# Kernel tuning notes

Measured on AMD Instinct MI355X. Metric: run time of the kernel, lower is better.

Reference implementation:

```python
import jax, jax.numpy as jnp
import numpy as np
from jax import lax

D_MODEL = 512
INPUT_DIM = 64
D_INNER = 1024      # expand * d_model
D_STATE = 128
NHEADS = 16         # d_inner // headdim (headdim = ssm_state//num_heads = 64)
HEADDIM = 64
D_CONV = 4
CONV_DIM = D_INNER + 2 * D_STATE          # 1280 (ngroups=1)
D_IN_PROJ = 2 * D_INNER + 2 * D_STATE + NHEADS  # 2320
BATCH = 2
SEQ = 1024
MASK_RATIO = 0.75
EPS = 1e-5


def setup_inputs() -> dict:
    key = jax.random.key(0)
    ks = jax.random.split(key, 14)
    s = lambda fan: 1.0 / np.sqrt(fan)
    return {
        "x": jax.random.normal(ks[0], (BATCH, SEQ, INPUT_DIM), jnp.float32),
        "conv_emb_w": jax.random.normal(ks[1], (D_MODEL, INPUT_DIM, 3), jnp.float32) * s(INPUT_DIM * 3),
        "conv_emb_b": jax.random.normal(ks[2], (D_MODEL,), jnp.float32) * 0.02,
        "cls_token": jax.random.normal(ks[3], (1, 1, D_MODEL), jnp.float32) * 0.02,
        "in_proj_w": jax.random.normal(ks[4], (D_IN_PROJ, D_MODEL), jnp.float32) * s(D_MODEL),
        "conv1d_w": jax.random.normal(ks[5], (CONV_DIM, 1, D_CONV), jnp.float32) * s(D_CONV),
        "conv1d_b": jax.random.normal(ks[6], (CONV_DIM,), jnp.float32) * 0.02,
        "dt_bias": jax.random.uniform(ks[7], (NHEADS,), jnp.float32, -4.0, 0.0),
        "A_log": jnp.log(jax.random.uniform(ks[8], (NHEADS,), jnp.float32, 1.0, 16.0)),
        "D": jax.random.normal(ks[9], (NHEADS,), jnp.float32),
        "rms_w": jnp.ones((D_INNER,), jnp.float32),
        "out_proj_w": jax.random.normal(ks[10], (D_MODEL, D_INNER), jnp.float32) * s(D_INNER),
        "ln_g": jnp.ones((D_MODEL,), jnp.float32),
        "ln_b": jnp.zeros((D_MODEL,), jnp.float32),
    }


def _forward(x, conv_emb_w, conv_emb_b, cls_token, in_proj_w, conv1d_w, conv1d_b,
             dt_bias, A_log, D, rms_w, out_proj_w, ln_g, ln_b):
    b = x.shape[0]
    # ---- conv embedding: Conv1d(k=3, pad=1) over time ----
    xe = lax.conv_general_dilated(x.transpose(0, 2, 1), conv_emb_w, (1,), [(1, 1)],
                                  dimension_numbers=("NCH", "OIH", "NCH"))
    xe = (xe + conv_emb_b[None, :, None]).transpose(0, 2, 1)  # (b, L, d_model)
    # ---- append CLS token at end ----
    h = jnp.concatenate([xe, jnp.broadcast_to(cls_token, (b, 1, D_MODEL))], axis=1)
    L = h.shape[1]
    # ---- Mamba2 block ----
    zxbcdt = jnp.einsum("bld,ed->ble", h, in_proj_w)  # (b, L, 2320)
    z = zxbcdt[..., :D_INNER]
    xBC = zxbcdt[..., D_INNER:D_INNER + CONV_DIM]
    dt = jax.nn.softplus(zxbcdt[..., -NHEADS:] + dt_bias)  # (b, L, h)
    # causal depthwise conv (pad left d_conv-1) + SiLU
    xBC = lax.conv_general_dilated(xBC.transpose(0, 2, 1), conv1d_w, (1,), [(D_CONV - 1, 0)],
                                   dimension_numbers=("NCH", "OIH", "NCH"),
                                   feature_group_count=CONV_DIM)
    xBC = jax.nn.silu((xBC + conv1d_b[None, :, None]).transpose(0, 2, 1))  # (b, L, 1280)
    x_in = xBC[..., :D_INNER].reshape(b, L, NHEADS, HEADDIM)   # (b, L, h, p)
    B = xBC[..., D_INNER:D_INNER + D_STATE]                     # (b, L, n)
    C = xBC[..., D_INNER + D_STATE:]                            # (b, L, n)
    A = -jnp.exp(A_log)                                         # (h,)
    dA = jnp.exp(dt * A)                                        # (b, L, h)
    # selective state-space scan; state (b, h, p, n)
    def step(state, inp):
        x_t, dt_t, B_t, C_t, dA_t = inp  # (b,h,p) (b,h) (b,n) (b,n) (b,h)
        state = state * dA_t[:, :, None, None] + \
            (dt_t[:, :, None] * x_t)[..., None] * B_t[:, None, None, :]
        y_t = jnp.einsum("bhpn,bn->bhp", state, C_t)
        return state, y_t
    s0 = jnp.zeros((b, NHEADS, HEADDIM, D_STATE), x.dtype)
    _, ys = lax.scan(step, s0, (x_in.transpose(1, 0, 2, 3), dt.transpose(1, 0, 2),
                                B.transpose(1, 0, 2), C.transpose(1, 0, 2),
                                dA.transpose(1, 0, 2)))
    y = ys.transpose(1, 0, 2, 3) + D[None, None, :, None] * x_in  # (b, L, h, p)
    y = y.reshape(b, L, D_INNER)
    # gated RMSNorm: gate first, then normalize
    y = y * jax.nn.silu(z)
    y = y * lax.rsqrt(jnp.mean(y * y, axis=-1, keepdims=True) + EPS) * rms_w
    out = jnp.einsum("ble,de->bld", y, out_proj_w)  # (b, L, d_model)
    # ---- LayerNorm ----
    mu = jnp.mean(out, axis=-1, keepdims=True)
    var = jnp.mean((out - mu) ** 2, axis=-1, keepdims=True)
    out = (out - mu) * lax.rsqrt(var + EPS) * ln_g + ln_b
    return out


def reference(x, conv_emb_w, conv_emb_b, cls_token, in_proj_w, conv1d_w, conv1d_b,
              dt_bias, A_log, D, rms_w, out_proj_w, ln_g, ln_b):
    out = _forward(x, conv_emb_w, conv_emb_b, cls_token, in_proj_w, conv1d_w, conv1d_b,
                   dt_bias, A_log, D, rms_w, out_proj_w, ln_g, ln_b)
    b = out.shape[0]
    cls = out[:, -1:, :]
    body = out[:, :-1, :]                      # (b, SEQ, d)
    len_keep = int(SEQ * (1 - MASK_RATIO))     # 256
    noise = jax.random.uniform(jax.random.fold_in(jax.random.key(0), 1), (b, SEQ))
    ids_shuffle = jnp.argsort(noise, axis=1)
    ids_restore = jnp.argsort(ids_shuffle, axis=1)
    ids_keep = ids_shuffle[:, :len_keep]
    x_masked = jnp.take_along_axis(body, ids_keep[:, :, None], axis=1)
    mask = jnp.where(jnp.arange(SEQ)[None, :] < len_keep, 0.0, 1.0)
    mask = jnp.take_along_axis(jnp.broadcast_to(mask, (b, SEQ)), ids_restore, axis=1)
    x_out = jnp.concatenate([x_masked, cls], axis=1)  # (b, len_keep+1, d)
    return (x_out, mask, ids_restore, ids_keep)
```

## Files before the change

kernel.cpp:

```cpp
#include <hip/hip_runtime.h>
#include <hip/hip_bf16.h>
#include <stdint.h>

#define LTOK  1025
#define NROWS 2050
#define DM    512
#define DIN   1024
#define DST   128
#define NHEAD 16
#define HDIM  64
#define CDIM  1280
#define EPROJ 2320
#define QC    64
#define NCH   17

#define O_RIDX   0
#define O_CB     1024
#define O_CLS    1536
#define O_C1B    2048
#define O_DTB    3328
#define O_ALOG   3344
#define O_DV     3360
#define O_RMSW   3376
#define O_LNG    4400
#define O_LNB    4912
#define O_CW     5440
#define O_IPW    103744
#define O_OPW    1291584
#define O_C1W    1815872
#define O_CX     1820992
#define O_ZX     1952064
#define O_XBC    6708064
#define O_DT     9332064
#define O_LGA    9364864
#define O_Y      9397664
#define O_X3     10447264
#define O_OUTG   11496864
#define O_SL     11760032
#define O_CLA    16216480
#define O_SL2    16251296
#define O_KEEP   18479520
#define O_OUTP   18480128
#define O_CWT    19532800
#define O_W2     19581952
#define O_BIAS2  19804672

#define OO_MASK 263168
#define OO_IDR  265216
#define OO_IDK  267264

typedef __attribute__((ext_vector_type(8))) short short8;
typedef __attribute__((ext_vector_type(8))) unsigned short ushortx8;
typedef __attribute__((ext_vector_type(4))) float floatx4;

__device__ __forceinline__ short f2bs(float f) {
  union { float f; uint32_t u; } v; v.f = f;
  uint32_t r = (v.u + 0x7FFFu + ((v.u >> 16) & 1u)) >> 16;
  return (short)r;
}
__device__ __forceinline__ float bf2f(uint16_t u) {
  return __uint_as_float(((uint32_t)u) << 16);
}

struct InPtrs { const void* p[14]; };

__device__ __forceinline__ uint32_t rotl32(uint32_t v, int d) {
  return (v << d) | (v >> (32 - d));
}
__device__ void threefry2x32(uint32_t k0, uint32_t k1, uint32_t c0, uint32_t c1,
                             uint32_t& o0, uint32_t& o1) {
  uint32_t ks0 = k0, ks1 = k1, ks2 = 0x1BD11BDAu ^ k0 ^ k1;
  uint32_t x0 = c0 + ks0, x1 = c1 + ks1;
#define TF_R4(a,b,c,d) \
  x0 += x1; x1 = rotl32(x1,a); x1 ^= x0; \
  x0 += x1; x1 = rotl32(x1,b); x1 ^= x0; \
  x0 += x1; x1 = rotl32(x1,c); x1 ^= x0; \
  x0 += x1; x1 = rotl32(x1,d); x1 ^= x0;
  TF_R4(13,15,26,6)  x0 += ks1; x1 += ks2 + 1u;
  TF_R4(17,29,16,24) x0 += ks2; x1 += ks0 + 2u;
  TF_R4(13,15,26,6)  x0 += ks0; x1 += ks1 + 3u;
  TF_R4(17,29,16,24) x0 += ks1; x1 += ks2 + 4u;
  TF_R4(13,15,26,6)  x0 += ks2; x1 += ks0 + 5u;
#undef TF_R4
  o0 = x0; o1 = x1;
}

__device__ int detect_is_f32(const uint32_t* w, int nelem) {
  int nw = nelem / 2; if (nw > 16) nw = 16;
  int insane = 0, lozero = 0, anynz = 0;
  for (int i = 0; i < nw; ++i) {
    uint32_t word = w[i];
    if (word != 0u) anynz = 1;
    uint32_t lo = word & 0xffffu;
    if (lo == 0u) { lozero++; continue; }
    float v = __uint_as_float(lo << 16);
    float a = fabsf(v);
    if (!(a >= 1e-8f && a <= 1e4f)) insane++;
  }
  if (insane >= 2) return 1;
  if (lozero == nw && anynz) return 1;
  return 0;
}

__global__ __launch_bounds__(256) void k_convert(InPtrs ptrs, float* ws,
                                                 float* out, int* rowidx) {
  static const int sizes[13] = {98304, 512, 512, 1187840, 5120, 1280,
                                16, 16, 16, 1024, 524288, 512, 512};
  static const int offs[13]  = {O_CW, O_CB, O_CLS, O_IPW, O_C1W, O_C1B,
                                O_DTB, O_ALOG, O_DV, O_RMSW, O_OPW, O_LNG, O_LNB};
  static const int isbf[13]  = {1,0,0,1,0,0,0,0,0,0,1,0,0};
  static const int smallT[15] = {1,2,4,4,4,4,4,5,5,6,7,8,9,11,12};
  static const int smallB[15] = {0,0,0,1,2,3,4,0,1,0,0,0,0,0,0};
  int bx = blockIdx.x;
  int tid = threadIdx.x;

  if (bx < 2048) {
    int b = bx >> 10, idx = bx & 1023;
    const uint32_t* xp = (const uint32_t*)ptrs.p[0];
    __shared__ int xf;
    if (tid == 0) xf = detect_is_f32(xp, 131072);
    __syncthreads();
    if (tid < 192) {
      int i = tid / 3, k = tid % 3;
      int tt = idx + k - 1;
      float v = 0.f;
      if (tt >= 0 && tt < 1024) {
        long src = ((long)(b * 1024 + tt)) * 64 + i;
        v = xf ? ((const float*)xp)[src] : bf2f(((const uint16_t*)xp)[src]);
      }
      ((uint16_t*)(ws + O_X3))[((long)(b * 1024 + idx)) * 192 + tid] = (uint16_t)f2bs(v);
    }
    return;
  }
  bx -= 2048;

  int t, blk;
  if (bx < 1160) { t = 3; blk = bx; }
  else {
    bx -= 1160;
    if (bx < 512) { t = 10; blk = bx; }
    else {
      bx -= 512;
      if (bx < 96) {
        const uint32_t* w = (const uint32_t*)ptrs.p[1];
        __shared__ int sf;
        if (tid == 0) sf = detect_is_f32(w, 98304);
        __syncthreads();
        int base = (bx * 256 + tid) * 4;
        if (base >= 98304) return;
        uint16_t vv[4];
        if (sf) {
          const float4 f = *(const float4*)((const float*)w + base);
          vv[0] = (uint16_t)f2bs(f.x); vv[1] = (uint16_t)f2bs(f.y);
          vv[2] = (uint16_t)f2bs(f.z); vv[3] = (uint16_t)f2bs(f.w);
        } else {
          const uint32_t* s = w + (base >> 1);
          uint32_t w0 = s[0], w1 = s[1];
          vv[0] = (uint16_t)(w0 & 0xffffu); vv[1] = (uint16_t)(w0 >> 16);
          vv[2] = (uint16_t)(w1 & 0xffffu); vv[3] = (uint16_t)(w1 >> 16);
        }
        int o = base / 192, ik = base % 192;
        uint16_t* cwt = (uint16_t*)(ws + O_CWT);
#pragma unroll
        for (int j = 0; j < 4; ++j)
          cwt[(long)(ik + j) * 512 + o] = vv[j];
        return;
      }
      bx -= 96;
      if (bx < 32) {
        int seg = bx & 15, b = bx >> 4;
        uint8_t* keep = (uint8_t*)(ws + O_KEEP);
        __shared__ float vals[1024];
        uint32_t fk0, fk1;
        threefry2x32(0u, 0u, 0u, 1u, fk0, fk1);
#pragma unroll
        for (int k = 0; k < 4; ++k) {
          int i = tid + k * 256;
          uint32_t o0, o1;
          threefry2x32(fk0, fk1, 0u, (uint32_t)(b * 1024 + i), o0, o1);
          uint32_t bits = o0 ^ o1;
          vals[i] = __uint_as_float((bits >> 9) | 0x3f800000u) - 1.0f;
        }
        __syncthreads();
        int tg = seg * 64 + (tid >> 2);
        int qq = tid & 3;
        float v = vals[tg];
        int r = 0;
        int j0 = qq * 256;
        for (int it = 0; it < 256; ++it) {
          int j = j0 + ((it + qq * 8) & 255);
          float vj = vals[j];
          r += (vj < v || (vj == v && j < tg)) ? 1 : 0;
        }
        r += __shfl_xor(r, 1, 64);
        r += __shfl_xor(r, 2, 64);
        if (qq == 0) {
          out[OO_IDR + b * 1024 + tg] = (float)r;
          out[OO_MASK + b * 1024 + tg] = (r < 256) ? 0.0f : 1.0f;
          keep[b * LTOK + tg] = (r < 256) ? 1 : 0;
          if (r < 256) {
            out[OO_IDK + b * 256 + r] = (float)tg;
            rowidx[b * 257 + r] = b * LTOK + tg;
          }
          if (tg == 0) {
            rowidx[b * 257 + 256] = b * LTOK + 1024;
            keep[b * LTOK + 1024] = 1;
          }
        }
        return;
      }
      bx -= 32;
      if (bx >= 15) return;
      t = smallT[bx]; blk = smallB[bx];
    }
  }

  int n = sizes[t];
  const uint32_t* w = (const uint32_t*)ptrs.p[t + 1];
  __shared__ int sf;
  if (tid == 0) sf = detect_is_f32(w, n);
  __syncthreads();
  int base = (blk * 256 + tid) * 4;
  if (base >= n) return;
  if (isbf[t]) {
    ushort4 o;
    if (sf) {
      const float4 vv = *(const float4*)((const float*)w + base);
      o.x = (uint16_t)f2bs(vv.x); o.y = (uint16_t)f2bs(vv.y);
      o.z = (uint16_t)f2bs(vv.z); o.w = (uint16_t)f2bs(vv.w);
    } else {
      const uint32_t* s = w + (base >> 1);
      uint32_t w0 = s[0], w1 = s[1];
      o.x = (uint16_t)(w0 & 0xffffu); o.y = (uint16_t)(w0 >> 16);
      o.z = (uint16_t)(w1 & 0xffffu); o.w = (uint16_t)(w1 >> 16);
    }
    *(ushort4*)((uint16_t*)(ws + offs[t]) + base) = o;
  } else {
    float* dst = ws + offs[t];
    if (sf) {
      *(float4*)(dst + base) = *(const float4*)((const float*)w + base);
    } else {
      const uint32_t* s = w + (base >> 1);
      uint32_t w0 = s[0], w1 = s[1];
      float4 o;
      o.x = __uint_as_float((w0 & 0xffffu) << 16);
      o.y = __uint_as_float(w0 & 0xffff0000u);
      o.z = __uint_as_float((w1 & 0xffffu) << 16);
      o.w = __uint_as_float(w1 & 0xffff0000u);
      *(float4*)(dst + base) = o;
    }
  }
}

__global__ __launch_bounds__(256) void k_w2(const uint16_t* __restrict__ IPW,
                                            const uint16_t* __restrict__ CWT,
                                            const float* __restrict__ cb,
                                            const float* __restrict__ cls,
                                            uint16_t* __restrict__ W2,
                                            float* __restrict__ bias2,
                                            uint16_t* __restrict__ ZX) {
  int bx = blockIdx.x;
  int tid = threadIdx.x;

  if (bx >= 111) {
    __shared__ float scb[512];
    __shared__ float scl[512];
    for (int i = tid; i < 512; i += 256) {
      scb[i] = cb[i];
      scl[i] = bf2f((uint16_t)f2bs(cls[i]));
    }
    __syncthreads();
    int e = (bx - 111) * 232 + tid;
    if (tid < 232 && e < 2320) {
      float sb = 0.f, sc = 0.f;
      for (int d8 = 0; d8 < 512; d8 += 8) {
        ushortx8 v = *(const ushortx8*)(IPW + (long)e * 512 + d8);
#pragma unroll
        for (int j = 0; j < 8; ++j) {
          float wv = bf2f(v[j]);
          sb = fmaf(wv, scb[d8 + j], sb);
          sc = fmaf(wv, scl[d8 + j], sc);
        }
      }
      bias2[e] = sb;
      uint16_t cz = (uint16_t)f2bs(sc);
      ZX[(long)1024 * EPROJ + e] = cz;
      ZX[(long)2049 * EPROJ + e] = cz;
    }
    return;
  }

  int bm = bx / 3, bn = bx % 3;
  __shared__ __align__(16) short sA[64 * 136];
  __shared__ __align__(16) short sB[64 * 136];
  int lane = tid & 63, w = tid >> 6, lm = lane & 15, q = lane >> 4;

  floatx4 acc[4] = {};
  for (int ph = 0; ph < 4; ++ph) {
    int d0 = ph * 128;
#pragma unroll
    for (int it = 0; it < 4; ++it) {
      int li = it * 256 + tid;
      int row = li >> 4, col = (li & 15) * 8;
      int ge = bm * 64 + row;
      ushortx8 av = {0,0,0,0,0,0,0,0};
      if (ge < 2320) av = *(const ushortx8*)(IPW + (long)ge * 512 + d0 + col);
      *(ushortx8*)&sA[row * 136 + col] = av;
      ushortx8 bv = *(const ushortx8*)(CWT + (long)(bn * 64 + row) * 512 + d0 + col);
      *(ushortx8*)&sB[row * 136 + col] = bv;
    }
    __syncthreads();
#pragma unroll
    for (int kk = 0; kk < 4; ++kk) {
      short8 a = *(const short8*)&sA[(w * 16 + lm) * 136 + kk * 32 + q * 8];
#pragma unroll
      for (int ct = 0; ct < 4; ++ct) {
        short8 b = *(const short8*)&sB[(ct * 16 + lm) * 136 + kk * 32 + q * 8];
        acc[ct] = __builtin_amdgcn_mfma_f32_16x16x32_bf16(a, b, acc[ct], 0, 0, 0);
      }
    }
    __syncthreads();
  }
#pragma unroll
  for (int reg = 0; reg < 4; ++reg) {
    int e = bm * 64 + w * 16 + q * 4 + reg;
    if (e < 2320) {
#pragma unroll
      for (int ct = 0; ct < 4; ++ct)
        W2[(long)e * 192 + bn * 64 + ct * 16 + lm] = (uint16_t)f2bs(acc[ct][reg]);
    }
  }
}

__global__ __launch_bounds__(256) void k_ipgemm(const uint16_t* __restrict__ X3,
                                                const uint16_t* __restrict__ W2,
                                                const float* __restrict__ bias2,
                                                uint16_t* __restrict__ ZX) {
  __shared__ __align__(16) short sA[64 * 200];
  __shared__ __align__(16) short sB[64 * 200];
  int tid = threadIdx.x;
  int lane = tid & 63, w = tid >> 6, lm = lane & 15, q = lane >> 4;
  int bm = blockIdx.y * 64, bn = blockIdx.x * 64;

#pragma unroll
  for (int it = 0; it < 6; ++it) {
    int li = it * 256 + tid;
    int row = li / 24, col = (li % 24) * 8;
    ushortx8 av = *(const ushortx8*)(X3 + (long)(bm + row) * 192 + col);
    *(ushortx8*)&sA[row * 200 + col] = av;
    int gn = bn + row;
    ushortx8 bv = {0,0,0,0,0,0,0,0};
    if (gn < 2320) bv = *(const ushortx8*)(W2 + (long)gn * 192 + col);
    *(ushortx8*)&sB[row * 200 + col] = bv;
  }
  __syncthreads();

  floatx4 acc[4] = {};
#pragma unroll
  for (int kb = 0; kb < 6; ++kb) {
    short8 a = *(const short8*)&sA[(w * 16 + lm) * 200 + kb * 32 + q * 8];
#pragma unroll
    for (int ct = 0; ct < 4; ++ct) {
      short8 b = *(const short8*)&sB[(ct * 16 + lm) * 200 + kb * 32 + q * 8];
      acc[ct] = __builtin_amdgcn_mfma_f32_16x16x32_bf16(a, b, acc[ct], 0, 0, 0);
    }
  }
#pragma unroll
  for (int reg = 0; reg < 4; ++reg) {
    int r = bm + w * 16 + q * 4 + reg;
    long crow = (long)((r >> 10) * LTOK + (r & 1023));
#pragma unroll
    for (int ct = 0; ct < 4; ++ct) {
      int e = bn + ct * 16 + lm;
      if (e < 2320)
        ZX[crow * EPROJ + e] = (uint16_t)f2bs(acc[ct][reg] + bias2[e]);
    }
  }
}

__global__ __launch_bounds__(256) void k_conv1d(const uint16_t* __restrict__ zx,
                                                const float* __restrict__ w,
                                                const float* __restrict__ bias,
                                                uint16_t* __restrict__ xbc,
                                                const float* __restrict__ dtb,
                                                const float* __restrict__ alog,
                                                float* __restrict__ dt,
                                                float* __restrict__ lga) {
  long rp_ = blockIdx.x;
  if (rp_ >= NROWS) {
    int idx = (int)(rp_ - NROWS) * 256 + threadIdx.x;
    if (idx < NROWS * NHEAD) {
      int rr = idx >> 4, h = idx & 15;
      float xv = bf2f(zx[(long)rr * EPROJ + (EPROJ - NHEAD) + h]) + dtb[h];
      float dtv = (xv > 20.f) ? xv : log1pf(expf(xv));
      dt[idx] = dtv;
      lga[idx] = dtv * (-expf(alog[h]));
    }
    return;
  }
  {
    int xcd = (int)(rp_ & 7), slot = (int)(rp_ >> 3);
    rp_ = (xcd < 2) ? (long)xcd * 257 + slot
                    : (long)514 + (long)(xcd - 2) * 256 + slot;
  }
  long r = rp_;
  int b = (int)(r / LTOK), t = (int)(r % LTOK);
  for (int c4 = threadIdx.x * 4; c4 < CDIM; c4 += 1024) {
    float4 bi = *(const float4*)(bias + c4);
    float a0 = bi.x, a1 = bi.y, a2 = bi.z, a3 = bi.w;
    float4 w0 = *(const float4*)(w + (c4 + 0) * 4);
    float4 w1 = *(const float4*)(w + (c4 + 1) * 4);
    float4 w2 = *(const float4*)(w + (c4 + 2) * 4);
    float4 w3 = *(const float4*)(w + (c4 + 3) * 4);
    float wr0[4] = {w0.x, w0.y, w0.z, w0.w};
    float wr1[4] = {w1.x, w1.y, w1.z, w1.w};
    float wr2[4] = {w2.x, w2.y, w2.z, w2.w};
    float wr3[4] = {w3.x, w3.y, w3.z, w3.w};
#pragma unroll
    for (int k = 0; k < 4; ++k) {
      int tt = t - 3 + k;
      if (tt >= 0) {
        ushort4 xv = *(const ushort4*)(zx + ((long)(b * LTOK + tt)) * EPROJ + DIN + c4);
        a0 = fmaf(wr0[k], bf2f(xv.x), a0);
        a1 = fmaf(wr1[k], bf2f(xv.y), a1);
        a2 = fmaf(wr2[k], bf2f(xv.z), a2);
        a3 = fmaf(wr3[k], bf2f(xv.w), a3);
      }
    }
    ushort4 o;
    o.x = (uint16_t)f2bs(a0 / (1.f + expf(-a0)));
    o.y = (uint16_t)f2bs(a1 / (1.f + expf(-a1)));
    o.z = (uint16_t)f2bs(a2 / (1.f + expf(-a2)));
    o.w = (uint16_t)f2bs(a3 / (1.f + expf(-a3)));
    *(ushort4*)(xbc + r * CDIM + c4) = o;
  }
}

__global__ __launch_bounds__(256) void k_ssd1(const uint16_t* __restrict__ xbc,
                                              const float* __restrict__ dt,
                                              const float* __restrict__ lga,
                                              float* __restrict__ SL,
                                              float* __restrict__ CLA) {
  int blk = blockIdx.x;
  int c = blk % NCH;
  int hh = blk / NCH;
  int h = hh & 15, b = hh >> 4;
  int tid = threadIdx.x;
  int lane = tid & 63, w = tid >> 6;
  int lm = lane & 15, q = lane >> 4;

  __shared__ __align__(16) short sBT[128 * 72];
  __shared__ __align__(16) short sXT[64 * 72];
  __shared__ float wwv[64];

  int t0 = c * QC;
  const uint16_t* base = xbc + (long)b * LTOK * CDIM;

  if (tid < 64) {
    int t = t0 + tid;
    float dtv = (t < LTOK) ? dt[((long)(b * LTOK + t)) * NHEAD + h] : 0.f;
    float v   = (t < LTOK) ? lga[((long)(b * LTOK + t)) * NHEAD + h] : 0.f;
#pragma unroll
    for (int off = 1; off < 64; off <<= 1) {
      float u = __shfl_up(v, off, 64);
      if (lane >= off) v += u;
    }
    float clEnd = __shfl(v, 63, 64);
    wwv[tid] = __expf(clEnd - v) * dtv;
    CLA[(long)blk * 64 + tid] = v;
  }
  __syncthreads();

#pragma unroll
  for (int k = 0; k < 8; ++k) {
    int e4 = (tid + k * 256) * 4;
    int row = e4 >> 7, col = e4 & 127;
    int t = t0 + row;
    ushort4 bv = {0,0,0,0};
    if (t < LTOK) bv = *(const ushort4*)(base + (long)t * CDIM + DIN + col);
    float wv = wwv[row];
    sBT[(col  )*72+row]=f2bs(bf2f(bv.x)*wv); sBT[(col+1)*72+row]=f2bs(bf2f(bv.y)*wv);
    sBT[(col+2)*72+row]=f2bs(bf2f(bv.z)*wv); sBT[(col+3)*72+row]=f2bs(bf2f(bv.w)*wv);
  }
#pragma unroll
  for (int k = 0; k < 4; ++k) {
    int e4 = (tid + k * 256) * 4;
    int row = e4 >> 6, col = e4 & 63;
    int t = t0 + row;
    ushort4 xv = {0,0,0,0};
    if (t < LTOK) xv = *(const ushort4*)(base + (long)t * CDIM + h * 64 + col);
    sXT[(col  )*72+row]=(short)xv.x; sXT[(col+1)*72+row]=(short)xv.y;
    sXT[(col+2)*72+row]=(short)xv.z; sXT[(col+3)*72+row]=(short)xv.w;
  }
  __syncthreads();

  floatx4 s[2][4] = {};
#pragma unroll
  for (int kb = 0; kb < 2; ++kb) {
    short8 bfr[4];
#pragma unroll
    for (int ct = 0; ct < 4; ++ct)
      bfr[ct] = *(const short8*)&sXT[(ct*16 + lm)*72 + kb*32 + q*8];
#pragma unroll
    for (int nt = 0; nt < 2; ++nt) {
      short8 a = *(const short8*)&sBT[((w*2+nt)*16 + lm)*72 + kb*32 + q*8];
#pragma unroll
      for (int ct = 0; ct < 4; ++ct)
        s[nt][ct] = __builtin_amdgcn_mfma_f32_16x16x32_bf16(a, bfr[ct], s[nt][ct], 0, 0, 0);
    }
  }
  float* slp = SL + (long)blk * 8192;
#pragma unroll
  for (int nt = 0; nt < 2; ++nt)
#pragma unroll
    for (int ct = 0; ct < 4; ++ct)
#pragma unroll
      for (int reg = 0; reg < 4; ++reg) {
        int n = (w*2+nt)*16 + q*4 + reg;
        int p = ct*16 + lm;
        slp[n*64 + p] = s[nt][ct][reg];
      }
}

__global__ __launch_bounds__(256) void k_comb(const float* __restrict__ SL,
                                              const float* __restrict__ CLA,
                                              uint16_t* __restrict__ SL2) {
  int bx = blockIdx.x;
  int piece = bx & 15;
  int hh = bx >> 4;
  int off = piece * 512 + threadIdx.x * 2;
  long cb0 = (long)hh * NCH;
  float P[NCH];
  float2 tmp[NCH];
#pragma unroll
  for (int c = 0; c < NCH; ++c) {
    P[c] = __expf(CLA[(cb0 + c) * 64 + 63]);
    tmp[c] = *(const float2*)(SL + (cb0 + c) * 8192 + off);
  }
  float2 s = make_float2(0.f, 0.f);
#pragma unroll
  for (int c = 0; c < NCH; ++c) {
    uint32_t packed = (uint32_t)(uint16_t)f2bs(s.x) | ((uint32_t)(uint16_t)f2bs(s.y) << 16);
    *(uint32_t*)(SL2 + (cb0 + c) * 8192 + off) = packed;
    s.x = fmaf(P[c], s.x, tmp[c].x);
    s.y = fmaf(P[c], s.y, tmp[c].y);
  }
}

__global__ __launch_bounds__(256) void k_ssd3(const uint16_t* __restrict__ xbc,
                                              const float* __restrict__ dt,
                                              const uint16_t* __restrict__ SL2,
                                              const float* __restrict__ CLA,
                                              const uint8_t* __restrict__ keepf,
                                              float* __restrict__ Y) {
  int blk = blockIdx.x;
  int c = blk % NCH;
  int hh = blk / NCH;
  int h = hh & 15, b = hh >> 4;
  int tid = threadIdx.x;
  int lane = tid & 63, w = tid >> 6;
  int lm = lane & 15, q = lane >> 4;

  __shared__ __align__(16) short sST[64 * 136];
  __shared__ __align__(16) short sXT[64 * 72];
  __shared__ __align__(16) short sM[64 * 72];
  __shared__ float dtw[64], clA[64], evec[64];
  __shared__ uint8_t kf[64];

  int t0 = c * QC;
  const uint16_t* base = xbc + (long)b * LTOK * CDIM;
  const uint16_t* slp = SL2 + (long)blk * 8192;

  if (tid < 64) {
    int t = t0 + tid;
    dtw[tid] = (t < LTOK) ? dt[((long)(b * LTOK + t)) * NHEAD + h] : 0.f;
    float v = CLA[(long)blk * 64 + tid];
    clA[tid] = v;
    evec[tid] = __expf(v);
    kf[tid] = (t < LTOK) ? keepf[b * LTOK + t] : 0;
  }

#pragma unroll
  for (int k = 0; k < 4; ++k) {
    int e4 = (tid + k * 256) * 4;
    int row = e4 >> 6, col = e4 & 63;
    int t = t0 + row;
    ushort4 xv = {0,0,0,0};
    if (t < LTOK) xv = *(const ushort4*)(base + (long)t * CDIM + h * 64 + col);
    sXT[(col  )*72+row]=(short)xv.x; sXT[(col+1)*72+row]=(short)xv.y;
    sXT[(col+2)*72+row]=(short)xv.z; sXT[(col+3)*72+row]=(short)xv.w;
  }
#pragma unroll
  for (int k = 0; k < 8; ++k) {
    int e4 = (tid + k * 256) * 4;
    int n = e4 >> 6, p = e4 & 63;
    ushort4 sv = *(const ushort4*)(slp + n * 64 + p);
    sST[(p  )*136+n]=(short)sv.x; sST[(p+1)*136+n]=(short)sv.y;
    sST[(p+2)*136+n]=(short)sv.z; sST[(p+3)*136+n]=(short)sv.w;
  }
  __syncthreads();

  short8 cfr[4];
  int tA = t0 + w*16 + lm;
  bool tAok = tA < LTOK;
#pragma unroll
  for (int kb = 0; kb < 4; ++kb) {
    short8 z = {0,0,0,0,0,0,0,0};
    cfr[kb] = tAok ? *(const short8*)(base + (long)tA * CDIM + DIN + DST + kb*32 + q*8) : z;
  }

  floatx4 g[4] = {};
#pragma unroll
  for (int kb = 0; kb < 4; ++kb) {
#pragma unroll
    for (int ct = 0; ct < 4; ++ct) {
      int tB = t0 + ct*16 + lm;
      short8 z = {0,0,0,0,0,0,0,0};
      short8 bb = (tB < LTOK) ? *(const short8*)(base + (long)tB * CDIM + DIN + kb*32 + q*8) : z;
      g[ct] = __builtin_amdgcn_mfma_f32_16x16x32_bf16(cfr[kb], bb, g[ct], 0, 0, 0);
    }
  }
#pragma unroll
  for (int ct = 0; ct < 4; ++ct) {
    int tp = ct*16 + lm;
#pragma unroll
    for (int reg = 0; reg < 4; ++reg) {
      int tl = w*16 + q*4 + reg;
      float m = 0.f;
      if (tp <= tl) m = g[ct][reg] * __expf(clA[tl] - clA[tp]) * dtw[tp];
      sM[tl*72 + tp] = f2bs(m);
    }
  }
  floatx4 y2[4] = {};
#pragma unroll
  for (int kb = 0; kb < 4; ++kb) {
#pragma unroll
    for (int ct = 0; ct < 4; ++ct) {
      short8 bb = *(const short8*)&sST[(ct*16 + lm)*136 + kb*32 + q*8];
      y2[ct] = __builtin_amdgcn_mfma_f32_16x16x32_bf16(cfr[kb], bb, y2[ct], 0, 0, 0);
    }
  }
  __syncthreads();
  floatx4 y1[4] = {};
#pragma unroll
  for (int kb = 0; kb < 2; ++kb) {
    short8 a = *(const short8*)&sM[(w*16 + lm)*72 + kb*32 + q*8];
#pragma unroll
    for (int ct = 0; ct < 4; ++ct) {
      short8 bb = *(const short8*)&sXT[(ct*16 + lm)*72 + kb*32 + q*8];
      y1[ct] = __builtin_amdgcn_mfma_f32_16x16x32_bf16(a, bb, y1[ct], 0, 0, 0);
    }
  }
#pragma unroll
  for (int reg = 0; reg < 4; ++reg) {
    int tl = w*16 + q*4 + reg;
    int t = t0 + tl;
    if (t < LTOK && kf[tl]) {
      float ev = evec[tl];
#pragma unroll
      for (int ct = 0; ct < 4; ++ct) {
        int p = ct*16 + lm;
        Y[((long)(b * LTOK + t)) * DIN + h * 64 + p] = y1[ct][reg] + ev * y2[ct][reg];
      }
    }
  }
}

__global__ __launch_bounds__(256) void k_gaterms(const float* __restrict__ Y,
                                                 const uint16_t* __restrict__ xbc,
                                                 const uint16_t* __restrict__ zx,
                                                 const float* __restrict__ Dv,
                                                 const float* __restrict__ rmsw,
                                                 const int* __restrict__ ridx,
                                                 uint16_t* __restrict__ G) {
  int rr = blockIdx.x;
  long r = ridx[rr];
  int tid = threadIdx.x;
  int e = tid * 4;
  int h = tid >> 4;
  float4 a = *(const float4*)(Y + r * DIN + e);
  const ushort4 xu = *(const ushort4*)(xbc + r * CDIM + e);
  const ushort4 zu = *(const ushort4*)(zx + r * EPROJ + e);
  float Dh = Dv[h];
  float y0 = a.x + Dh * bf2f(xu.x), y1 = a.y + Dh * bf2f(xu.y);
  float y2 = a.z + Dh * bf2f(xu.z), y3 = a.w + Dh * bf2f(xu.w);
  float z0 = bf2f(zu.x), z1 = bf2f(zu.y), z2 = bf2f(zu.z), z3 = bf2f(zu.w);
  float g0 = y0 * (z0 / (1.f + expf(-z0)));
  float g1 = y1 * (z1 / (1.f + expf(-z1)));
  float g2 = y2 * (z2 / (1.f + expf(-z2)));
  float g3 = y3 * (z3 / (1.f + expf(-z3)));
  __shared__ float red[256];
  red[tid] = g0*g0 + g1*g1 + g2*g2 + g3*g3;
  __syncthreads();
  for (int st = 128; st; st >>= 1) {
    if (tid < st) red[tid] += red[tid + st];
    __syncthreads();
  }
  float scale = rsqrtf(red[0] * (1.0f / 1024.0f) + 1e-5f);
  float4 rw = *(const float4*)(rmsw + e);
  ushort4 o;
  o.x = (uint16_t)f2bs(g0 * scale * rw.x);
  o.y = (uint16_t)f2bs(g1 * scale * rw.y);
  o.z = (uint16_t)f2bs(g2 * scale * rw.z);
  o.w = (uint16_t)f2bs(g3 * scale * rw.w);
  *(ushort4*)(G + (long)rr * DIN + e) = o;
}

__global__ __launch_bounds__(256) void k_ogemm(const uint16_t* __restrict__ A,
                                               const uint16_t* __restrict__ Bw,
                                               float* __restrict__ OUTP) {
  __shared__ __align__(16) short sA[64 * 264];
  __shared__ __align__(16) short sB[64 * 264];
  int tid = threadIdx.x;
  int lane = tid & 63, w = tid >> 6;
  int lm = lane & 15, q = lane >> 4;
  int bm = blockIdx.y * 64, bn = blockIdx.x * 64;
  int kbase = blockIdx.z * 256;

#pragma unroll
  for (int it = 0; it < 8; ++it) {
    int li = it * 256 + tid;
    int row = li >> 5, col = (li & 31) * 8;
    int gm = bm + row;
    ushortx8 av = {0,0,0,0,0,0,0,0};
    if (gm < 514) av = *(const ushortx8*)(A + (long)gm * 1024 + kbase + col);
    *(ushortx8*)&sA[row * 264 + col] = av;
    ushortx8 bv = *(const ushortx8*)(Bw + (long)(bn + row) * 1024 + kbase + col);
    *(ushortx8*)&sB[row * 264 + col] = bv;
  }
  __syncthreads();

  floatx4 acc[4] = {};
#pragma unroll
  for (int kb = 0; kb < 8; ++kb) {
    short8 a = *(const short8*)&sA[(w * 16 + lm) * 264 + kb * 32 + q * 8];
#pragma unroll
    for (int ct = 0; ct < 4; ++ct) {
      short8 b = *(const short8*)&sB[(ct * 16 + lm) * 264 + kb * 32 + q * 8];
      acc[ct] = __builtin_amdgcn_mfma_f32_16x16x32_bf16(a, b, acc[ct], 0, 0, 0);
    }
  }
  float* op = OUTP + (long)blockIdx.z * 263168;
#pragma unroll
  for (int reg = 0; reg < 4; ++reg) {
    int r = bm + w * 16 + q * 4 + reg;
    if (r < 514) {
#pragma unroll
      for (int ct = 0; ct < 4; ++ct)
        op[(long)r * 512 + bn + ct * 16 + lm] = acc[ct][reg];
    }
  }
}

__global__ __launch_bounds__(256) void k_ln(const float* __restrict__ outp,
                                            const float* __restrict__ lng,
                                            const float* __restrict__ lnb,
                                            float* __restrict__ out) {
  int r = blockIdx.x;
  int tid = threadIdx.x;
  long e = (long)r * DM + tid * 2;
  float2 v0 = *(const float2*)(outp + e);
  float2 v1 = *(const float2*)(outp + 263168 + e);
  float2 v2 = *(const float2*)(outp + 2 * 263168 + e);
  float2 v3 = *(const float2*)(outp + 3 * 263168 + e);
  float2 v;
  v.x = ((v0.x + v1.x) + v2.x) + v3.x;
  v.y = ((v0.y + v1.y) + v2.y) + v3.y;
  __shared__ float red[256];
  red[tid] = v.x + v.y;
  __syncthreads();
  for (int st = 128; st; st >>= 1) { if (tid < st) red[tid] += red[tid + st]; __syncthreads(); }
  float mu = red[0] * (1.0f / 512.0f);
  __syncthreads();
  float dx = v.x - mu, dy = v.y - mu;
  red[tid] = dx * dx + dy * dy;
  __syncthreads();
  for (int st = 128; st; st >>= 1) { if (tid < st) red[tid] += red[tid + st]; __syncthreads(); }
  float sc = rsqrtf(red[0] * (1.0f / 512.0f) + 1e-5f);
  int c = tid * 2;
  out[(long)r * DM + c]     = dx * sc * lng[c] + lnb[c];
  out[(long)r * DM + c + 1] = dy * sc * lng[c + 1] + lnb[c + 1];
}

extern "C" void kernel_launch(void* const* d_in, const int* in_sizes, int n_in,
                              void* d_out, int out_size, void* d_ws, size_t ws_size,
                              hipStream_t stream) {
  float* ws = (float*)d_ws;
  float* out = (float*)d_out;
  int* rowidx = (int*)(ws + O_RIDX);
  InPtrs ip;
  for (int i = 0; i < 14; ++i) ip.p[i] = d_in[i];

  hipLaunchKernelGGL(k_convert, dim3(3863), dim3(256), 0, stream, ip, ws, out, rowidx);
  hipLaunchKernelGGL(k_w2, dim3(121), dim3(256), 0, stream,
                     (const uint16_t*)(ws + O_IPW), (const uint16_t*)(ws + O_CWT),
                     ws + O_CB, ws + O_CLS,
                     (uint16_t*)(ws + O_W2), ws + O_BIAS2, (uint16_t*)(ws + O_ZX));
  hipLaunchKernelGGL(k_ipgemm, dim3(37, 32), dim3(256), 0, stream,
                     (const uint16_t*)(ws + O_X3), (const uint16_t*)(ws + O_W2),
                     ws + O_BIAS2, (uint16_t*)(ws + O_ZX));
  hipLaunchKernelGGL(k_conv1d, dim3(2179), dim3(256), 0, stream,
                     (const uint16_t*)(ws + O_ZX), ws + O_C1W, ws + O_C1B,
                     (uint16_t*)(ws + O_XBC),
                     ws + O_DTB, ws + O_ALOG, ws + O_DT, ws + O_LGA);
  hipLaunchKernelGGL(k_ssd1, dim3(32 * NCH), dim3(256), 0, stream,
                     (const uint16_t*)(ws + O_XBC), ws + O_DT, ws + O_LGA,
                     ws + O_SL, ws + O_CLA);
  hipLaunchKernelGGL(k_comb, dim3(512), dim3(256), 0, stream,
                     ws + O_SL, ws + O_CLA, (uint16_t*)(ws + O_SL2));
  hipLaunchKernelGGL(k_ssd3, dim3(32 * NCH), dim3(256), 0, stream,
                     (const uint16_t*)(ws + O_XBC), ws + O_DT,
                     (const uint16_t*)(ws + O_SL2), ws + O_CLA,
                     (const uint8_t*)(ws + O_KEEP), ws + O_Y);
  hipLaunchKernelGGL(k_gaterms, dim3(514), dim3(256), 0, stream,
                     ws + O_Y, (const uint16_t*)(ws + O_XBC),
                     (const uint16_t*)(ws + O_ZX), ws + O_DV, ws + O_RMSW,
                     (const int*)rowidx, (uint16_t*)(ws + O_X3));
  hipLaunchKernelGGL(k_ogemm, dim3(8, 9, 4), dim3(256), 0, stream,
                     (const uint16_t*)(ws + O_X3), (const uint16_t*)(ws + O_OPW),
                     ws + O_OUTP);
  hipLaunchKernelGGL(k_ln, dim3(514), dim3(256), 0, stream,
                     ws + O_OUTP, ws + O_LNG, ws + O_LNB, out);
}
```

Measured before the change: 191.1 us.

## Fuse input/weight dtype conversion into consuming GEMM loads, shrink convert kernel

Stops converting in_proj, out_proj weights and building the im2col X3 buffer in the convert kernel. Instead the w2, input-projection GEMM and output GEMM kernels read the raw inputs and convert to bf16 on load. The conv-embedding weight transpose is permuted so the im2col column order matches contiguous 8-element loads. This removes thousands of convert blocks and a round trip through workspace, at the cost of every block re-running the dtype detection and, with f32 inputs, reading twice the bytes per GEMM tile.

```diff
diff --git a/kernel.cpp b/kernel.cpp
--- a/kernel.cpp
+++ b/kernel.cpp
@@ -102,6 +102,22 @@
   return 0;
 }
 
+__device__ __forceinline__ ushortx8 load8_bf16(const void* src, long idx, int isf32) {
+  ushortx8 r;
+  if (isf32) {
+    const float* p = (const float*)src + idx;
+    float4 f0 = *(const float4*)p;
+    float4 f1 = *(const float4*)(p + 4);
+    r[0] = (uint16_t)f2bs(f0.x); r[1] = (uint16_t)f2bs(f0.y);
+    r[2] = (uint16_t)f2bs(f0.z); r[3] = (uint16_t)f2bs(f0.w);
+    r[4] = (uint16_t)f2bs(f1.x); r[5] = (uint16_t)f2bs(f1.y);
+    r[6] = (uint16_t)f2bs(f1.z); r[7] = (uint16_t)f2bs(f1.w);
+  } else {
+    r = *(const ushortx8*)((const uint16_t*)src + idx);
+  }
+  return r;
+}
+
 __global__ __launch_bounds__(256) void k_convert(InPtrs ptrs, float* ws,
                                                  float* out, int* rowidx) {
   static const int sizes[13] = {98304, 512, 512, 1187840, 5120, 1280,
@@ -114,106 +130,80 @@
   int bx = blockIdx.x;
   int tid = threadIdx.x;
 
-  if (bx < 2048) {
-    int b = bx >> 10, idx = bx & 1023;
-    const uint32_t* xp = (const uint32_t*)ptrs.p[0];
-    __shared__ int xf;
-    if (tid == 0) xf = detect_is_f32(xp, 131072);
+  if (bx < 96) {
+    const uint32_t* w = (const uint32_t*)ptrs.p[1];
+    __shared__ int sf;
+    if (tid == 0) sf = detect_is_f32(w, 98304);
     __syncthreads();
-    if (tid < 192) {
-      int i = tid / 3, k = tid % 3;
-      int tt = idx + k - 1;
-      float v = 0.f;
-      if (tt >= 0 && tt < 1024) {
-        long src = ((long)(b * 1024 + tt)) * 64 + i;
-        v = xf ? ((const float*)xp)[src] : bf2f(((const uint16_t*)xp)[src]);
+    int base = (bx * 256 + tid) * 4;
+    if (base >= 98304) return;
+    uint16_t vv[4];
+    if (sf) {
+      const float4 f = *(const float4*)((const float*)w + base);
+      vv[0] = (uint16_t)f2bs(f.x); vv[1] = (uint16_t)f2bs(f.y);
+      vv[2] = (uint16_t)f2bs(f.z); vv[3] = (uint16_t)f2bs(f.w);
+    } else {
+      const uint32_t* s = w + (base >> 1);
+      uint32_t w0 = s[0], w1 = s[1];
+      vv[0] = (uint16_t)(w0 & 0xffffu); vv[1] = (uint16_t)(w0 >> 16);
+      vv[2] = (uint16_t)(w1 & 0xffffu); vv[3] = (uint16_t)(w1 >> 16);
+    }
+    int o = base / 192, ik = base % 192;
+    uint16_t* cwt = (uint16_t*)(ws + O_CWT);
+#pragma unroll
+    for (int j = 0; j < 4; ++j) {
+      int ikj = ik + j;
+      int kp = (ikj % 3) * 64 + (ikj / 3);
+      cwt[(long)kp * 512 + o] = vv[j];
+    }
+    return;
+  }
+  bx -= 96;
+  if (bx < 32) {
+    int seg = bx & 15, b = bx >> 4;
+    uint8_t* keep = (uint8_t*)(ws + O_KEEP);
+    __shared__ float vals[1024];
+    uint32_t fk0, fk1;
+    threefry2x32(0u, 0u, 0u, 1u, fk0, fk1);
+#pragma unroll
+    for (int k = 0; k < 4; ++k) {
+      int i = tid + k * 256;
+      uint32_t o0, o1;
+      threefry2x32(fk0, fk1, 0u, (uint32_t)(b * 1024 + i), o0, o1);
+      uint32_t bits = o0 ^ o1;
+      vals[i] = __uint_as_float((bits >> 9) | 0x3f800000u) - 1.0f;
+    }
+    __syncthreads();
+    int tg = seg * 64 + (tid >> 2);
+    int qq = tid & 3;
+    float v = vals[tg];
+    int r = 0;
+    int j0 = qq * 256;
+    for (int it = 0; it < 256; ++it) {
+      int j = j0 + ((it + qq * 8) & 255);
+      float vj = vals[j];
+      r += (vj < v || (vj == v && j < tg)) ? 1 : 0;
+    }
+    r += __shfl_xor(r, 1, 64);
+    r += __shfl_xor(r, 2, 64);
+    if (qq == 0) {
+      out[OO_IDR + b * 1024 + tg] = (float)r;
+      out[OO_MASK + b * 1024 + tg] = (r < 256) ? 0.0f : 1.0f;
+      keep[b * LTOK + tg] = (r < 256) ? 1 : 0;
+      if (r < 256) {
+        out[OO_IDK + b * 256 + r] = (float)tg;
+        rowidx[b * 257 + r] = b * LTOK + tg;
       }
-      ((uint16_t*)(ws + O_X3))[((long)(b * 1024 + idx)) * 192 + tid] = (uint16_t)f2bs(v);
+      if (tg == 0) {
+        rowidx[b * 257 + 256] = b * LTOK + 1024;
+        keep[b * LTOK + 1024] = 1;
+      }
     }
     return;
   }
-  bx -= 2048;
-
-  int t, blk;
-  if (bx < 1160) { t = 3; blk = bx; }
-  else {
-    bx -= 1160;
-    if (bx < 512) { t = 10; blk = bx; }
-    else {
-      bx -= 512;
-      if (bx < 96) {
-        const uint32_t* w = (const uint32_t*)ptrs.p[1];
-        __shared__ int sf;
-        if (tid == 0) sf = detect_is_f32(w, 98304);
-        __syncthreads();
-        int base = (bx * 256 + tid) * 4;
-        if (base >= 98304) return;
-        uint16_t vv[4];
-        if (sf) {
-          const float4 f = *(const float4*)((const float*)w + base);
-          vv[0] = (uint16_t)f2bs(f.x); vv[1] = (uint16_t)f2bs(f.y);
-          vv[2] = (uint16_t)f2bs(f.z); vv[3] = (uint16_t)f2bs(f.w);
-        } else {
-          const uint32_t* s = w + (base >> 1);
-          uint32_t w0 = s[0], w1 = s[1];
-          vv[0] = (uint16_t)(w0 & 0xffffu); vv[1] = (uint16_t)(w0 >> 16);
-          vv[2] = (uint16_t)(w1 & 0xffffu); vv[3] = (uint16_t)(w1 >> 16);
-        }
-        int o = base / 192, ik = base % 192;
-        uint16_t* cwt = (uint16_t*)(ws + O_CWT);
-#pragma unroll
-        for (int j = 0; j < 4; ++j)
-          cwt[(long)(ik + j) * 512 + o] = vv[j];
-        return;
-      }
-      bx -= 96;
-      if (bx < 32) {
-        int seg = bx & 15, b = bx >> 4;
-        uint8_t* keep = (uint8_t*)(ws + O_KEEP);
-        __shared__ float vals[1024];
-        uint32_t fk0, fk1;
-        threefry2x32(0u, 0u, 0u, 1u, fk0, fk1);
-#pragma unroll
-        for (int k = 0; k < 4; ++k) {
-          int i = tid + k * 256;
-          uint32_t o0, o1;
-          threefry2x32(fk0, fk1, 0u, (uint32_t)(b * 1024 + i), o0, o1);
-          uint32_t bits = o0 ^ o1;
-          vals[i] = __uint_as_float((bits >> 9) | 0x3f800000u) - 1.0f;
-        }
-        __syncthreads();
-        int tg = seg * 64 + (tid >> 2);
-        int qq = tid & 3;
-        float v = vals[tg];
-        int r = 0;
-        int j0 = qq * 256;
-        for (int it = 0; it < 256; ++it) {
-          int j = j0 + ((it + qq * 8) & 255);
-          float vj = vals[j];
-          r += (vj < v || (vj == v && j < tg)) ? 1 : 0;
-        }
-        r += __shfl_xor(r, 1, 64);
-        r += __shfl_xor(r, 2, 64);
-        if (qq == 0) {
-          out[OO_IDR + b * 1024 + tg] = (float)r;
-          out[OO_MASK + b * 1024 + tg] = (r < 256) ? 0.0f : 1.0f;
-          keep[b * LTOK + tg] = (r < 256) ? 1 : 0;
-          if (r < 256) {
-            out[OO_IDK + b * 256 + r] = (float)tg;
-            rowidx[b * 257 + r] = b * LTOK + tg;
-          }
-          if (tg == 0) {
-            rowidx[b * 257 + 256] = b * LTOK + 1024;
-            keep[b * LTOK + 1024] = 1;
-          }
-        }
-        return;
-      }
-      bx -= 32;
-      if (bx >= 15) return;
-      t = smallT[bx]; blk = smallB[bx];
-    }
-  }
+  bx -= 32;
+  if (bx >= 15) return;
+  int t = smallT[bx], blk = smallB[bx];
 
   int n = sizes[t];
   const uint32_t* w = (const uint32_t*)ptrs.p[t + 1];
@@ -252,7 +242,7 @@
   }
 }
 
-__global__ __launch_bounds__(256) void k_w2(const uint16_t* __restrict__ IPW,
+__global__ __launch_bounds__(256) void k_w2(const void* __restrict__ IPWr,
                                             const uint16_t* __restrict__ CWT,
                                             const float* __restrict__ cb,
                                             const float* __restrict__ cls,
@@ -261,6 +251,8 @@
                                             uint16_t* __restrict__ ZX) {
   int bx = blockIdx.x;
   int tid = threadIdx.x;
+  __shared__ int sf;
+  if (tid == 0) sf = detect_is_f32((const uint32_t*)IPWr, 1187840);
 
   if (bx >= 111) {
     __shared__ float scb[512];
@@ -274,7 +266,7 @@
     if (tid < 232 && e < 2320) {
       float sb = 0.f, sc = 0.f;
       for (int d8 = 0; d8 < 512; d8 += 8) {
-        ushortx8 v = *(const ushortx8*)(IPW + (long)e * 512 + d8);
+        ushortx8 v = load8_bf16(IPWr, (long)e * 512 + d8, sf);
 #pragma unroll
         for (int j = 0; j < 8; ++j) {
           float wv = bf2f(v[j]);
@@ -294,6 +286,7 @@
   __shared__ __align__(16) short sA[64 * 136];
   __shared__ __align__(16) short sB[64 * 136];
   int lane = tid & 63, w = tid >> 6, lm = lane & 15, q = lane >> 4;
+  __syncthreads();
 
   floatx4 acc[4] = {};
   for (int ph = 0; ph < 4; ++ph) {
@@ -304,7 +297,7 @@
       int row = li >> 4, col = (li & 15) * 8;
       int ge = bm * 64 + row;
       ushortx8 av = {0,0,0,0,0,0,0,0};
-      if (ge < 2320) av = *(const ushortx8*)(IPW + (long)ge * 512 + d0 + col);
+      if (ge < 2320) av = load8_bf16(IPWr, (long)ge * 512 + d0 + col, sf);
       *(ushortx8*)&sA[row * 136 + col] = av;
       ushortx8 bv = *(const ushortx8*)(CWT + (long)(bn * 64 + row) * 512 + d0 + col);
       *(ushortx8*)&sB[row * 136 + col] = bv;
@@ -332,7 +325,7 @@
   }
 }
 
-__global__ __launch_bounds__(256) void k_ipgemm(const uint16_t* __restrict__ X3,
+__global__ __launch_bounds__(256) void k_ipgemm(const void* __restrict__ xraw,
                                                 const uint16_t* __restrict__ W2,
                                                 const float* __restrict__ bias2,
                                                 uint16_t* __restrict__ ZX) {
@@ -341,17 +334,26 @@
   int tid = threadIdx.x;
   int lane = tid & 63, w = tid >> 6, lm = lane & 15, q = lane >> 4;
   int bm = blockIdx.y * 64, bn = blockIdx.x * 64;
+  __shared__ int xf;
+  if (tid == 0) xf = detect_is_f32((const uint32_t*)xraw, 131072);
+  __syncthreads();
 
 #pragma unroll
   for (int it = 0; it < 6; ++it) {
     int li = it * 256 + tid;
-    int row = li / 24, col = (li % 24) * 8;
-    ushortx8 av = *(const ushortx8*)(X3 + (long)(bm + row) * 192 + col);
-    *(ushortx8*)&sA[row * 200 + col] = av;
+    int row = li / 24, colb = (li % 24) * 8;
+    int r = bm + row;
+    int b = r >> 10, idx = r & 1023;
+    int kk = colb >> 6, i0 = colb & 63;
+    int tt = idx + kk - 1;
+    ushortx8 av = {0,0,0,0,0,0,0,0};
+    if (tt >= 0 && tt < 1024)
+      av = load8_bf16(xraw, ((long)(b * 1024 + tt)) * 64 + i0, xf);
+    *(ushortx8*)&sA[row * 200 + colb] = av;
     int gn = bn + row;
     ushortx8 bv = {0,0,0,0,0,0,0,0};
-    if (gn < 2320) bv = *(const ushortx8*)(W2 + (long)gn * 192 + col);
-    *(ushortx8*)&sB[row * 200 + col] = bv;
+    if (gn < 2320) bv = *(const ushortx8*)(W2 + (long)gn * 192 + colb);
+    *(ushortx8*)&sB[row * 200 + colb] = bv;
   }
   __syncthreads();
 
@@ -707,7 +709,7 @@
 }
 
 __global__ __launch_bounds__(256) void k_ogemm(const uint16_t* __restrict__ A,
-                                               const uint16_t* __restrict__ Bw,
+                                               const void* __restrict__ OPWr,
                                                float* __restrict__ OUTP) {
   __shared__ __align__(16) short sA[64 * 264];
   __shared__ __align__(16) short sB[64 * 264];
@@ -716,6 +718,9 @@
   int lm = lane & 15, q = lane >> 4;
   int bm = blockIdx.y * 64, bn = blockIdx.x * 64;
   int kbase = blockIdx.z * 256;
+  __shared__ int of;
+  if (tid == 0) of = detect_is_f32((const uint32_t*)OPWr, 524288);
+  __syncthreads();
 
 #pragma unroll
   for (int it = 0; it < 8; ++it) {
@@ -725,7 +730,7 @@
     ushortx8 av = {0,0,0,0,0,0,0,0};
     if (gm < 514) av = *(const ushortx8*)(A + (long)gm * 1024 + kbase + col);
     *(ushortx8*)&sA[row * 264 + col] = av;
-    ushortx8 bv = *(const ushortx8*)(Bw + (long)(bn + row) * 1024 + kbase + col);
+    ushortx8 bv = load8_bf16(OPWr, (long)(bn + row) * 1024 + kbase + col, of);
     *(ushortx8*)&sB[row * 264 + col] = bv;
   }
   __syncthreads();
@@ -791,13 +796,13 @@
   InPtrs ip;
   for (int i = 0; i < 14; ++i) ip.p[i] = d_in[i];
 
-  hipLaunchKernelGGL(k_convert, dim3(3863), dim3(256), 0, stream, ip, ws, out, rowidx);
+  hipLaunchKernelGGL(k_convert, dim3(143), dim3(256), 0, stream, ip, ws, out, rowidx);
   hipLaunchKernelGGL(k_w2, dim3(121), dim3(256), 0, stream,
-                     (const uint16_t*)(ws + O_IPW), (const uint16_t*)(ws + O_CWT),
+                     (const void*)d_in[4], (const uint16_t*)(ws + O_CWT),
                      ws + O_CB, ws + O_CLS,
                      (uint16_t*)(ws + O_W2), ws + O_BIAS2, (uint16_t*)(ws + O_ZX));
   hipLaunchKernelGGL(k_ipgemm, dim3(37, 32), dim3(256), 0, stream,
-                     (const uint16_t*)(ws + O_X3), (const uint16_t*)(ws + O_W2),
+                     (const void*)d_in[0], (const uint16_t*)(ws + O_W2),
                      ws + O_BIAS2, (uint16_t*)(ws + O_ZX));
   hipLaunchKernelGGL(k_conv1d, dim3(2179), dim3(256), 0, stream,
                      (const uint16_t*)(ws + O_ZX), ws + O_C1W, ws + O_C1B,
@@ -817,7 +822,7 @@
                      (const uint16_t*)(ws + O_ZX), ws + O_DV, ws + O_RMSW,
                      (const int*)rowidx, (uint16_t*)(ws + O_X3));
   hipLaunchKernelGGL(k_ogemm, dim3(8, 9, 4), dim3(256), 0, stream,
-                     (const uint16_t*)(ws + O_X3), (const uint16_t*)(ws + O_OPW),
+                     (const uint16_t*)(ws + O_X3), (const void*)d_in[11],
                      ws + O_OUTP);
   hipLaunchKernelGGL(k_ln, dim3(514), dim3(256), 0, stream,
                      ws + O_OUTP, ws + O_LNG, ws + O_LNB, out);
```

Result: slower. 208.4 us (+9.0%).

## Skip z-gate stores for masked rows and tile conv1d over four timesteps

Applied to the files above, without the earlier changes.

The in-projection GEMM epilogue now reads a per-row keep mask and skips writing the z (gate) columns for rows that are later discarded, which cuts global store traffic. The depthwise conv1d kernel now computes four consecutive timesteps per block and reuses the seven loaded input rows across the 4-tap windows, instead of reloading four rows for every output row. This shrinks the grid from one block per row to one per four rows. The trade-off is more registers per thread and fewer blocks to fill the device.

```diff
diff --git a/kernel.cpp b/kernel.cpp
--- a/kernel.cpp
+++ b/kernel.cpp
@@ -335,13 +335,19 @@
 __global__ __launch_bounds__(256) void k_ipgemm(const uint16_t* __restrict__ X3,
                                                 const uint16_t* __restrict__ W2,
                                                 const float* __restrict__ bias2,
+                                                const uint8_t* __restrict__ keep,
                                                 uint16_t* __restrict__ ZX) {
   __shared__ __align__(16) short sA[64 * 200];
   __shared__ __align__(16) short sB[64 * 200];
+  __shared__ uint8_t skp[64];
   int tid = threadIdx.x;
   int lane = tid & 63, w = tid >> 6, lm = lane & 15, q = lane >> 4;
   int bm = blockIdx.y * 64, bn = blockIdx.x * 64;
 
+  if (tid < 64) {
+    int rr = bm + tid;
+    skp[tid] = keep[(rr >> 10) * LTOK + (rr & 1023)];
+  }
 #pragma unroll
   for (int it = 0; it < 6; ++it) {
     int li = it * 256 + tid;
@@ -369,10 +375,11 @@
   for (int reg = 0; reg < 4; ++reg) {
     int r = bm + w * 16 + q * 4 + reg;
     long crow = (long)((r >> 10) * LTOK + (r & 1023));
+    int kp = skp[r - bm];
 #pragma unroll
     for (int ct = 0; ct < 4; ++ct) {
       int e = bn + ct * 16 + lm;
-      if (e < 2320)
+      if (e < 2320 && (e >= DIN || kp))
         ZX[crow * EPROJ + e] = (uint16_t)f2bs(acc[ct][reg] + bias2[e]);
     }
   }
@@ -386,9 +393,10 @@
                                                 const float* __restrict__ alog,
                                                 float* __restrict__ dt,
                                                 float* __restrict__ lga) {
-  long rp_ = blockIdx.x;
-  if (rp_ >= NROWS) {
-    int idx = (int)(rp_ - NROWS) * 256 + threadIdx.x;
+  int g = blockIdx.x;
+  int tid = threadIdx.x;
+  if (g >= 514) {
+    int idx = (g - 514) * 256 + tid;
     if (idx < NROWS * NHEAD) {
       int rr = idx >> 4, h = idx & 15;
       float xv = bf2f(zx[(long)rr * EPROJ + (EPROJ - NHEAD) + h]) + dtb[h];
@@ -399,40 +407,55 @@
     return;
   }
   {
-    int xcd = (int)(rp_ & 7), slot = (int)(rp_ >> 3);
-    rp_ = (xcd < 2) ? (long)xcd * 257 + slot
-                    : (long)514 + (long)(xcd - 2) * 256 + slot;
-  }
-  long r = rp_;
-  int b = (int)(r / LTOK), t = (int)(r % LTOK);
-  for (int c4 = threadIdx.x * 4; c4 < CDIM; c4 += 1024) {
+    int xcd = g & 7, slot = g >> 3;
+    g = (xcd < 2) ? xcd * 65 + slot : 130 + (xcd - 2) * 64 + slot;
+  }
+  int b = g / 257, gi = g % 257;
+  int t0 = gi * 4;
+  int nr = (t0 == 1024) ? 1 : 4;
+  const uint16_t* zrow = zx + (long)b * LTOK * EPROJ + DIN;
+  for (int c4 = tid * 4; c4 < CDIM; c4 += 1024) {
     float4 bi = *(const float4*)(bias + c4);
-    float a0 = bi.x, a1 = bi.y, a2 = bi.z, a3 = bi.w;
     float4 w0 = *(const float4*)(w + (c4 + 0) * 4);
     float4 w1 = *(const float4*)(w + (c4 + 1) * 4);
     float4 w2 = *(const float4*)(w + (c4 + 2) * 4);
     float4 w3 = *(const float4*)(w + (c4 + 3) * 4);
-    float wr0[4] = {w0.x, w0.y, w0.z, w0.w};
-    float wr1[4] = {w1.x, w1.y, w1.z, w1.w};
-    float wr2[4] = {w2.x, w2.y, w2.z, w2.w};
-    float wr3[4] = {w3.x, w3.y, w3.z, w3.w};
-#pragma unroll
-    for (int k = 0; k < 4; ++k) {
-      int tt = t - 3 + k;
-      if (tt >= 0) {
-        ushort4 xv = *(const ushort4*)(zx + ((long)(b * LTOK + tt)) * EPROJ + DIN + c4);
-        a0 = fmaf(wr0[k], bf2f(xv.x), a0);
-        a1 = fmaf(wr1[k], bf2f(xv.y), a1);
-        a2 = fmaf(wr2[k], bf2f(xv.z), a2);
-        a3 = fmaf(wr3[k], bf2f(xv.w), a3);
+    float wr[4][4] = {{w0.x, w0.y, w0.z, w0.w}, {w1.x, w1.y, w1.z, w1.w},
+                      {w2.x, w2.y, w2.z, w2.w}, {w3.x, w3.y, w3.z, w3.w}};
+    float acc[4][4];
+#pragma unroll
+    for (int ri = 0; ri < 4; ++ri) {
+      acc[ri][0] = bi.x; acc[ri][1] = bi.y; acc[ri][2] = bi.z; acc[ri][3] = bi.w;
+    }
+#pragma unroll
+    for (int dtt = -3; dtt <= 3; ++dtt) {
+      int tt = t0 + dtt;
+      if (tt < 0 || tt > 1024) continue;
+      ushort4 xv = *(const ushort4*)(zrow + (long)tt * EPROJ + c4);
+      float x0 = bf2f(xv.x), x1 = bf2f(xv.y), x2 = bf2f(xv.z), x3 = bf2f(xv.w);
+#pragma unroll
+      for (int ri = 0; ri < 4; ++ri) {
+        int k = dtt - ri + 3;
+        if (k >= 0 && k <= 3) {
+          acc[ri][0] = fmaf(wr[0][k], x0, acc[ri][0]);
+          acc[ri][1] = fmaf(wr[1][k], x1, acc[ri][1]);
+          acc[ri][2] = fmaf(wr[2][k], x2, acc[ri][2]);
+          acc[ri][3] = fmaf(wr[3][k], x3, acc[ri][3]);
+        }
       }
     }
-    ushort4 o;
-    o.x = (uint16_t)f2bs(a0 / (1.f + expf(-a0)));
-    o.y = (uint16_t)f2bs(a1 / (1.f + expf(-a1)));
-    o.z = (uint16_t)f2bs(a2 / (1.f + expf(-a2)));
-    o.w = (uint16_t)f2bs(a3 / (1.f + expf(-a3)));
-    *(ushort4*)(xbc + r * CDIM + c4) = o;
+#pragma unroll
+    for (int ri = 0; ri < 4; ++ri) {
+      if (ri < nr) {
+        long r = (long)b * LTOK + t0 + ri;
+        ushort4 o;
+        o.x = (uint16_t)f2bs(acc[ri][0] / (1.f + expf(-acc[ri][0])));
+        o.y = (uint16_t)f2bs(acc[ri][1] / (1.f + expf(-acc[ri][1])));
+        o.z = (uint16_t)f2bs(acc[ri][2] / (1.f + expf(-acc[ri][2])));
+        o.w = (uint16_t)f2bs(acc[ri][3] / (1.f + expf(-acc[ri][3])));
+        *(ushort4*)(xbc + r * CDIM + c4) = o;
+      }
+    }
   }
 }
 
@@ -798,8 +821,9 @@
                      (uint16_t*)(ws + O_W2), ws + O_BIAS2, (uint16_t*)(ws + O_ZX));
   hipLaunchKernelGGL(k_ipgemm, dim3(37, 32), dim3(256), 0, stream,
                      (const uint16_t*)(ws + O_X3), (const uint16_t*)(ws + O_W2),
-                     ws + O_BIAS2, (uint16_t*)(ws + O_ZX));
-  hipLaunchKernelGGL(k_conv1d, dim3(2179), dim3(256), 0, stream,
+                     ws + O_BIAS2, (const uint8_t*)(ws + O_KEEP),
+                     (uint16_t*)(ws + O_ZX));
+  hipLaunchKernelGGL(k_conv1d, dim3(643), dim3(256), 0, stream,
                      (const uint16_t*)(ws + O_ZX), ws + O_C1W, ws + O_C1B,
                      (uint16_t*)(ws + O_XBC),
                      ws + O_DTB, ws + O_ALOG, ws + O_DT, ws + O_LGA);
```

New measurement: 186.9 us. -2.2%, faster.
